# Optimization experiments

Measured on AMD Instinct MI355X. Metric: run time of the kernel, lower is better.

## Reference

```python
import jax, jax.numpy as jnp
import numpy as np

BLOCK_SIZE = 64          # elements per quantization block
SCALER_BLOCK_SIZE = 256  # scalers per double-quantization block
OUT, IN = 11008, 4096
N_BLOCKS = OUT * IN // BLOCK_SIZE          # 704512
N_SCALER_BLOCKS = N_BLOCKS // SCALER_BLOCK_SIZE  # 2752

# QLoRA NF4 (4-bit NormalFloat) codebook
NF4_TABLE = np.array([
    -1.0, -0.6961928009986877, -0.5250730514526367, -0.39491748809814453,
    -0.28444138169288635, -0.18477343022823334, -0.10644006729125977,
    -0.029167551919817924, 0.0, 0.07958029955625534, 0.16093020141124725,
    0.24611230194568634, 0.33791524171829224, 0.44070982933044434,
    0.5626170039176941, 0.7229568362236023], dtype=np.float32)


def setup_inputs() -> dict:
    key = jax.random.key(0)
    k1, k2, k3, k4, k5 = jax.random.split(key, 5)
    x = jax.random.normal(k1, (4, 2048, IN), dtype=jnp.float32)
    # 4-bit codebook indices for each weight element
    qweight = jax.random.randint(k2, (OUT, IN), 0, 16, dtype=jnp.int32)
    # int8-style quantized per-block scalers (positive magnitudes)
    quantized_scalers = jax.random.randint(k3, (N_BLOCKS,), 1, 127, dtype=jnp.int32)
    # per scaler-block quantization factor (strictly positive, away from zero)
    quantization_factor = jax.random.uniform(k4, (N_SCALER_BLOCKS,), dtype=jnp.float32,
                                             minval=0.5, maxval=1.5) * 127.0
    scaler_mean = jax.random.uniform(k5, (1,), dtype=jnp.float32) * 0.01
    return {"x": x, "qweight": qweight, "quantized_scalers": quantized_scalers,
            "quantization_factor": quantization_factor, "scaler_mean": scaler_mean}


def dequantize_nf4(qweight, quantized_scalers, quantization_factor, scaler_mean, dtype):
    table = jnp.asarray(NF4_TABLE, dtype=dtype)
    # double-dequantize the per-block scalers
    scalers = (quantized_scalers.astype(dtype)
               / jnp.repeat(quantization_factor.astype(dtype), SCALER_BLOCK_SIZE)
               + scaler_mean.astype(dtype)[0])                      # [N_BLOCKS]
    # codebook lookup, then per-block scale
    w = table[qweight].reshape(N_BLOCKS, BLOCK_SIZE) * scalers[:, None]
    return w.reshape(OUT, IN)


def reference(x, qweight, quantized_scalers, quantization_factor, scaler_mean):
    # Faithful to LinearNF4.forward: F.linear(x, weight.to(x.dtype))
    w = dequantize_nf4(qweight, quantized_scalers, quantization_factor,
                       scaler_mean, x.dtype)                        # [OUT, IN]
    return jnp.einsum('bsi,oi->bso', x, w)
```

## Files before the change

### kernel.cpp

```cpp
#include <hip/hip_runtime.h>
#include <stdint.h>

#define M_ROWS 8192
#define K_DIM  4096
#define N_DIM  11008
#define KSTEPS (K_DIM / 64)

#define BM 256
#define BN 256
#define MBLKS (M_ROWS / BM)
#define NBLKS (N_DIM / BN)
#define NWG   (MBLKS * NBLKS)

typedef __attribute__((ext_vector_type(4))) float          f32x4;
typedef __attribute__((ext_vector_type(8))) __bf16         bf16x8;
typedef __attribute__((ext_vector_type(4))) int            i32x4;
typedef __attribute__((ext_vector_type(8))) unsigned short u16x8;

__constant__ float NF4_TBL[16] = {
    -1.0f, -0.6961928009986877f, -0.5250730514526367f, -0.39491748809814453f,
    -0.28444138169288635f, -0.18477343022823334f, -0.10644006729125977f,
    -0.029167551919817924f, 0.0f, 0.07958029955625534f, 0.16093020141124725f,
    0.24611230194568634f, 0.33791524171829224f, 0.44070982933044434f,
    0.5626170039176941f, 0.7229568362236023f};

__device__ __forceinline__ unsigned short f2bf(float f) {
  uint32_t u = __float_as_uint(f);
  u += 0x7fffu + ((u >> 16) & 1u);
  return (unsigned short)(u >> 16);
}

__device__ __forceinline__ void gload_lds16(const void* g, const void* l) {
  __builtin_amdgcn_global_load_lds(
      (const __attribute__((address_space(1))) void*)(uintptr_t)g,
      (__attribute__((address_space(3))) void*)(uint32_t)(uintptr_t)l,
      16, 0, 0);
}

__global__ void convert_x_kernel(const float* __restrict__ x,
                                 unsigned short* __restrict__ xb) {
  const long n8 = (long)M_ROWS * K_DIM / 8;
  for (long t = (long)blockIdx.x * blockDim.x + threadIdx.x; t < n8;
       t += (long)gridDim.x * blockDim.x) {
    const float* p = x + t * 8;
    f32x4 v0 = *(const f32x4*)p;
    f32x4 v1 = *(const f32x4*)(p + 4);
    u16x8 o;
    o[0] = f2bf(v0[0]); o[1] = f2bf(v0[1]); o[2] = f2bf(v0[2]); o[3] = f2bf(v0[3]);
    o[4] = f2bf(v1[0]); o[5] = f2bf(v1[1]); o[6] = f2bf(v1[2]); o[7] = f2bf(v1[3]);
    *(u16x8*)(xb + t * 8) = o;
  }
}

__global__ void dequant_w_kernel(const int* __restrict__ qw,
                                 const int* __restrict__ qs,
                                 const float* __restrict__ qf,
                                 const float* __restrict__ mean,
                                 unsigned short* __restrict__ wb) {
  __shared__ float tbl[16];
  if (threadIdx.x < 16) tbl[threadIdx.x] = NF4_TBL[threadIdx.x];
  __syncthreads();
  const float mu = mean[0];
  const long n8 = (long)N_DIM * K_DIM / 8;
  for (long t = (long)blockIdx.x * blockDim.x + threadIdx.x; t < n8;
       t += (long)gridDim.x * blockDim.x) {
    long f = t * 8;
    int  g = (int)(f >> 6);
    float s = (float)qs[g] / qf[g >> 8] + mu;
    i32x4 q0 = *(const i32x4*)(qw + f);
    i32x4 q1 = *(const i32x4*)(qw + f + 4);
    u16x8 o;
    o[0] = f2bf(tbl[q0[0]] * s); o[1] = f2bf(tbl[q0[1]] * s);
    o[2] = f2bf(tbl[q0[2]] * s); o[3] = f2bf(tbl[q0[3]] * s);
    o[4] = f2bf(tbl[q1[0]] * s); o[5] = f2bf(tbl[q1[1]] * s);
    o[6] = f2bf(tbl[q1[2]] * s); o[7] = f2bf(tbl[q1[3]] * s);
    *(u16x8*)(wb + f) = o;
  }
}

#define STG(GP, LB)                                                              \
  gload_lds16((GP) + (long)srow * K_DIM + scol, &LDSbuf[(LB) + wid * 1024]);     \
  gload_lds16((GP) + (long)(64 + srow) * K_DIM + scol,                           \
              &LDSbuf[(LB) + 8192 + wid * 1024]);

#define SB __builtin_amdgcn_sched_barrier(0)

#define RD_A2(DST, MB, SA)                                                        \
  DST[0][0] = *(const bf16x8*)&LDSbuf[(SA) + aoff + (MB) * 2048 + kswz0];         \
  DST[0][1] = *(const bf16x8*)&LDSbuf[(SA) + aoff + (MB) * 2048 + kswz1];         \
  DST[1][0] = *(const bf16x8*)&LDSbuf[(SA) + aoff + ((MB) + 1) * 2048 + kswz0];   \
  DST[1][1] = *(const bf16x8*)&LDSbuf[(SA) + aoff + ((MB) + 1) * 2048 + kswz1];

#define RD_B2(NB, CB)                                                             \
  bq[NB][0]     = *(const bf16x8*)&LDSbuf[(CB) + boff + (NB) * 2048 + kswz0];     \
  bq[NB][1]     = *(const bf16x8*)&LDSbuf[(CB) + boff + (NB) * 2048 + kswz1];     \
  bq[NB + 1][0] = *(const bf16x8*)&LDSbuf[(CB) + boff + ((NB) + 1) * 2048 + kswz0];\
  bq[NB + 1][1] = *(const bf16x8*)&LDSbuf[(CB) + boff + ((NB) + 1) * 2048 + kswz1];

#define MFP(MI, AF, AI, NI)                                                       \
  acc[MI][NI] = __builtin_amdgcn_mfma_f32_16x16x32_bf16(AF[AI][0], bq[NI][0], acc[MI][NI], 0, 0, 0); \
  acc[MI][NI] = __builtin_amdgcn_mfma_f32_16x16x32_bf16(AF[AI][1], bq[NI][1], acc[MI][NI], 0, 0, 0);

#define TILE_BODY(BASE)                                                           \
    RD_B2(0, cB);                                                                 \
    SB;                                                                           \
    RD_B2(2, cB);                                                                 \
    STG(wb + n0g * K_DIM + kB, nB);                                               \
    __builtin_amdgcn_s_setprio(1);                                                \
    MFP(((BASE) + 0) & 7, af_a, 0, 0) MFP(((BASE) + 1) & 7, af_a, 1, 0)           \
    MFP(((BASE) + 0) & 7, af_a, 0, 1) MFP(((BASE) + 1) & 7, af_a, 1, 1)           \
    __builtin_amdgcn_s_setprio(0);                                                \
    SB;                                                                           \
    RD_A2(af_b, ((BASE) + 2) & 7, sAr);                                           \
    STG(wb + (n0g + 128) * K_DIM + kB, nB + 16384);                               \
    __builtin_amdgcn_s_setprio(1);                                                \
    MFP(((BASE) + 0) & 7, af_a, 0, 2) MFP(((BASE) + 1) & 7, af_a, 1, 2)           \
    MFP(((BASE) + 0) & 7, af_a, 0, 3) MFP(((BASE) + 1) & 7, af_a, 1, 3)           \
    __builtin_amdgcn_s_setprio(0);                                                \
    SB;                                                                           \
    STG(xb + m0g * K_DIM + kA, sAs);                                              \
    __builtin_amdgcn_s_setprio(1);                                                \
    MFP(((BASE) + 2) & 7, af_b, 0, 2) MFP(((BASE) + 3) & 7, af_b, 1, 2)           \
    MFP(((BASE) + 2) & 7, af_b, 0, 3) MFP(((BASE) + 3) & 7, af_b, 1, 3)           \
    __builtin_amdgcn_s_setprio(0);                                                \
    SB;                                                                           \
    RD_A2(af_a, ((BASE) + 4) & 7, sAr);                                           \
    STG(xb + (m0g + 128) * K_DIM + kA, sAs + 16384);                              \
    __builtin_amdgcn_s_setprio(1);                                                \
    MFP(((BASE) + 2) & 7, af_b, 0, 0) MFP(((BASE) + 3) & 7, af_b, 1, 0)           \
    MFP(((BASE) + 2) & 7, af_b, 0, 1) MFP(((BASE) + 3) & 7, af_b, 1, 1)           \
    __builtin_amdgcn_s_setprio(0);                                                \
    SB;                                                                           \
    __builtin_amdgcn_s_setprio(1);                                                \
    MFP(((BASE) + 4) & 7, af_a, 0, 0) MFP(((BASE) + 5) & 7, af_a, 1, 0)           \
    MFP(((BASE) + 4) & 7, af_a, 0, 1) MFP(((BASE) + 5) & 7, af_a, 1, 1)           \
    __builtin_amdgcn_s_setprio(0);                                                \
    SB;                                                                           \
    RD_A2(af_b, ((BASE) + 6) & 7, sAr);                                           \
    __builtin_amdgcn_s_setprio(1);                                                \
    MFP(((BASE) + 4) & 7, af_a, 0, 2) MFP(((BASE) + 5) & 7, af_a, 1, 2)           \
    MFP(((BASE) + 4) & 7, af_a, 0, 3) MFP(((BASE) + 5) & 7, af_a, 1, 3)           \
    __builtin_amdgcn_s_setprio(0);                                                \
    SB;                                                                           \
    RD_A2(af_a, ((BASE) + 0) & 7, sAn);          \
    __builtin_amdgcn_s_setprio(1);                                                \
    MFP(((BASE) + 6) & 7, af_b, 0, 2) MFP(((BASE) + 7) & 7, af_b, 1, 2)           \
    MFP(((BASE) + 6) & 7, af_b, 0, 3) MFP(((BASE) + 7) & 7, af_b, 1, 3)           \
    __builtin_amdgcn_s_setprio(0);                                                \
    SB;                                                                           \
    __builtin_amdgcn_s_setprio(1);                                                \
    MFP(((BASE) + 6) & 7, af_b, 0, 0) MFP(((BASE) + 7) & 7, af_b, 1, 0)           \
    MFP(((BASE) + 6) & 7, af_b, 0, 1) MFP(((BASE) + 7) & 7, af_b, 1, 1)           \
    __builtin_amdgcn_s_setprio(0);

#define TILE_SETUP                                                                \
    const int cur = t & 1;                                                        \
    const int cB = 98304 + cur * 32768;                                           \
    const int nB = 98304 + (cur ^ 1) * 32768;                                     \
    const long kB = (long)((t + 1 < KSTEPS ? t + 1 : KSTEPS - 1) * 64);           \
    const long kA = (long)((t + 2 < KSTEPS ? t + 2 : KSTEPS - 1) * 64);

#define TILE_BOUND                                                                \
    asm volatile("s_waitcnt vmcnt(4)");                                           \
    __builtin_amdgcn_sched_barrier(0);                                            \
    __builtin_amdgcn_s_barrier();                                                 \
    __builtin_amdgcn_sched_barrier(0);                                            \
    int tmp = sAr; sAr = sAn; sAn = sAs; sAs = tmp;

__global__ __launch_bounds__(512, 2) void gemm_pipe(
    const unsigned short* __restrict__ xb, const unsigned short* __restrict__ wb,
    float* __restrict__ C) {
  __align__(16) __shared__ unsigned char LDSbuf[163840];

  const int tid = threadIdx.x;
  const int wid = tid >> 6, lane = tid & 63;
  const int wr = wid >> 2, wc = wid & 3;
  const int r16 = lane & 15, hi = lane >> 4;

  const int p = ((int)blockIdx.x & 7) * (NWG / 8) + ((int)blockIdx.x >> 3);
  int mb, nb;
  if (p < 1280) {
    const int nbg = p >> 7;
    const int rem = p & 127;
    const int mbg = rem >> 5;
    const int s   = rem & 31;
    mb = mbg * 8 + (s & 7);
    nb = nbg * 4 + (s >> 3);
  } else {
    const int q   = p - 1280;
    const int mbg = q / 24;
    const int s   = q % 24;
    mb = mbg * 8 + (s & 7);
    nb = 40 + (s >> 3);
  }
  const long m0g = (long)mb * BM, n0g = (long)nb * BN;

  const int srow = wid * 8 + (lane >> 3);
  const int scol = ((lane & 7) ^ (lane >> 3)) * 8;

  const int aoff = (wr * 128 + r16) * 128;
  const int boff = (wc * 64 + r16) * 128;
  const int kswz0 = ((hi ^ (r16 & 7)) << 4);
  const int kswz1 = kswz0 ^ 64;

  STG(xb + m0g * K_DIM,              0);
  STG(xb + (m0g + 128) * K_DIM,      16384);
  STG(wb + n0g * K_DIM,              98304);
  STG(wb + (n0g + 128) * K_DIM,      98304 + 16384);
  STG(xb + m0g * K_DIM + 64,         32768);
  STG(xb + (m0g + 128) * K_DIM + 64, 32768 + 16384);
  asm volatile("s_waitcnt vmcnt(4)");
  __builtin_amdgcn_sched_barrier(0);
  __builtin_amdgcn_s_barrier();

  bf16x8 af_a[2][2], af_b[2][2], bq[4][2];
  f32x4 acc[8][4] = {};

  int sAr = 0, sAn = 32768, sAs = 65536;

  if ((wid & 1) == 0) {
    RD_A2(af_a, 0, sAr);
    for (int t = 0; t < KSTEPS; ++t) {
      TILE_SETUP
      TILE_BODY(0)
      TILE_BOUND
    }
  } else {
    RD_A2(af_a, 4, sAr);
    for (int t = 0; t < KSTEPS; ++t) {
      TILE_SETUP
      TILE_BODY(4)
      TILE_BOUND
    }
  }

  const long crow = m0g + wr * 128 + hi * 4;
  const long ccol = n0g + wc * 64 + r16;
#pragma unroll
  for (int m = 0; m < 8; ++m)
#pragma unroll
    for (int n = 0; n < 4; ++n)
#pragma unroll
      for (int r = 0; r < 4; ++r)
        __builtin_nontemporal_store(
            acc[m][n][r], &C[(crow + m * 16 + r) * N_DIM + ccol + n * 16]);
}

__global__ __launch_bounds__(256) void gemm_fallback(
    const float* __restrict__ Xf, const int* __restrict__ qw,
    const int* __restrict__ qs, const float* __restrict__ qf,
    const float* __restrict__ meanp, float* __restrict__ C) {
  __shared__ unsigned short As[128 * 64];
  __shared__ unsigned short Bs[128 * 64];
  __shared__ float tbl[16];
  const int tid = threadIdx.x;
  if (tid < 16) tbl[tid] = NF4_TBL[tid];
  const float mu = meanp[0];
  const int nwg = (M_ROWS / 128) * (N_DIM / 128);
  const int wg = ((int)blockIdx.x & 7) * (nwg / 8) + ((int)blockIdx.x >> 3);
  const int mbf = wg % (M_ROWS / 128), nbf = wg / (M_ROWS / 128);
  const int m0 = mbf * 128, n0 = nbf * 128;
  const int wid = tid >> 6, lane = tid & 63;
  const int wrf = wid >> 1, wcc = wid & 1;
  const int r16 = lane & 15, hi = lane >> 4;
  f32x4 acc[4][4] = {};
  for (int t = 0; t < KSTEPS; ++t) {
    const int k0 = t * 64;
    __syncthreads();
#pragma unroll
    for (int i = 0; i < 4; ++i) {
      int gi = i * 256 + tid;
      int row = gi >> 3, kq = (gi & 7) * 8;
      const float* px = Xf + (long)(m0 + row) * K_DIM + k0 + kq;
      f32x4 v0 = *(const f32x4*)px;
      f32x4 v1 = *(const f32x4*)(px + 4);
      u16x8 o;
      o[0] = f2bf(v0[0]); o[1] = f2bf(v0[1]); o[2] = f2bf(v0[2]); o[3] = f2bf(v0[3]);
      o[4] = f2bf(v1[0]); o[5] = f2bf(v1[1]); o[6] = f2bf(v1[2]); o[7] = f2bf(v1[3]);
      *(u16x8*)&As[row * 64 + kq] = o;
    }
#pragma unroll
    for (int i = 0; i < 4; ++i) {
      int gi = i * 256 + tid;
      int row = gi >> 3, kq = (gi & 7) * 8;
      const int* pq = qw + (long)(n0 + row) * K_DIM + k0 + kq;
      i32x4 q0 = *(const i32x4*)pq;
      i32x4 q1 = *(const i32x4*)(pq + 4);
      int g = (n0 + row) * (K_DIM / 64) + t;
      float s = (float)qs[g] / qf[g >> 8] + mu;
      u16x8 o;
      o[0] = f2bf(tbl[q0[0]] * s); o[1] = f2bf(tbl[q0[1]] * s);
      o[2] = f2bf(tbl[q0[2]] * s); o[3] = f2bf(tbl[q0[3]] * s);
      o[4] = f2bf(tbl[q1[0]] * s); o[5] = f2bf(tbl[q1[1]] * s);
      o[6] = f2bf(tbl[q1[2]] * s); o[7] = f2bf(tbl[q1[3]] * s);
      *(u16x8*)&Bs[row * 64 + kq] = o;
    }
    __syncthreads();
    bf16x8 afr[4][2], bfr[4][2];
#pragma unroll
    for (int i = 0; i < 4; ++i)
#pragma unroll
      for (int h = 0; h < 2; ++h) {
        afr[i][h] = *(const bf16x8*)&As[(wrf * 64 + i * 16 + r16) * 64 + h * 32 + hi * 8];
        bfr[i][h] = *(const bf16x8*)&Bs[(wcc * 64 + i * 16 + r16) * 64 + h * 32 + hi * 8];
      }
#pragma unroll
    for (int i = 0; i < 4; ++i)
#pragma unroll
      for (int j = 0; j < 4; ++j) {
        acc[i][j] = __builtin_amdgcn_mfma_f32_16x16x32_bf16(afr[i][0], bfr[j][0], acc[i][j], 0, 0, 0);
        acc[i][j] = __builtin_amdgcn_mfma_f32_16x16x32_bf16(afr[i][1], bfr[j][1], acc[i][j], 0, 0, 0);
      }
  }
  const int crow = m0 + wrf * 64 + hi * 4;
  const int ccol = n0 + wcc * 64 + r16;
#pragma unroll
  for (int i = 0; i < 4; ++i)
#pragma unroll
    for (int j = 0; j < 4; ++j)
#pragma unroll
      for (int r = 0; r < 4; ++r)
        C[(long)(crow + i * 16 + r) * N_DIM + (ccol + j * 16)] = acc[i][j][r];
}

extern "C" void kernel_launch(void* const* d_in, const int* in_sizes, int n_in,
                              void* d_out, int out_size, void* d_ws, size_t ws_size,
                              hipStream_t stream) {
  const float* x    = (const float*)d_in[0];
  const int*   qw   = (const int*)d_in[1];
  const int*   qs   = (const int*)d_in[2];
  const float* qf   = (const float*)d_in[3];
  const float* mean = (const float*)d_in[4];
  float* out = (float*)d_out;

  const size_t xb_bytes = (size_t)M_ROWS * K_DIM * 2;
  const size_t wb_bytes = (size_t)N_DIM * K_DIM * 2;

  if (ws_size >= xb_bytes + wb_bytes) {
    unsigned short* xb = (unsigned short*)d_ws;
    unsigned short* wb = (unsigned short*)((char*)d_ws + xb_bytes);
    convert_x_kernel<<<4096, 256, 0, stream>>>(x, xb);
    dequant_w_kernel<<<4096, 256, 0, stream>>>(qw, qs, qf, mean, wb);
    gemm_pipe<<<NWG, 512, 0, stream>>>(xb, wb, out);
  } else {
    gemm_fallback<<<(M_ROWS / 128) * (N_DIM / 128), 256, 0, stream>>>(
        x, qw, qs, qf, mean, out);
  }
}
```

Measured before the change: 687.9 us.

## Split-K the tail tiles of the GEMM to balance the last wave

The 96 tiles in the last column group (nb 40-42) are each split along K into two halves, giving 1472 workgroups instead of 1376. The second half writes its partial sums to a workspace buffer, and a new fixup kernel adds them into the output. The aim is to cut the idle time of a partially filled final wave across the CUs. In exchange it adds an extra kernel launch and extra memory traffic for the partial tiles, and it only runs when the workspace is large enough.

Result: no change. 685.2 us (-0.4%).

```diff
diff --git a/kernel.cpp b/kernel.cpp
--- a/kernel.cpp
+++ b/kernel.cpp
@@ -11,6 +11,7 @@
 #define MBLKS (M_ROWS / BM)
 #define NBLKS (N_DIM / BN)
 #define NWG   (MBLKS * NBLKS)
+#define NWG_SPLIT 1472
 
 typedef __attribute__((ext_vector_type(4))) float          f32x4;
 typedef __attribute__((ext_vector_type(8))) __bf16         bf16x8;
@@ -157,8 +158,8 @@
     const int cur = t & 1;                                                        \
     const int cB = 98304 + cur * 32768;                                           \
     const int nB = 98304 + (cur ^ 1) * 32768;                                     \
-    const long kB = (long)((t + 1 < KSTEPS ? t + 1 : KSTEPS - 1) * 64);           \
-    const long kA = (long)((t + 2 < KSTEPS ? t + 2 : KSTEPS - 1) * 64);
+    const long kB = (long)((t + 1 < tend ? t + 1 : tend - 1) * 64);               \
+    const long kA = (long)((t + 2 < tend ? t + 2 : tend - 1) * 64);
 
 #define TILE_BOUND                                                                \
     asm volatile("s_waitcnt vmcnt(4)");                                           \
@@ -167,9 +168,10 @@
     __builtin_amdgcn_sched_barrier(0);                                            \
     int tmp = sAr; sAr = sAn; sAn = sAs; sAs = tmp;
 
+template <bool SPLIT>
 __global__ __launch_bounds__(512, 2) void gemm_pipe(
     const unsigned short* __restrict__ xb, const unsigned short* __restrict__ wb,
-    float* __restrict__ C) {
+    float* __restrict__ C, float* __restrict__ P) {
   __align__(16) __shared__ unsigned char LDSbuf[163840];
 
   const int tid = threadIdx.x;
@@ -177,21 +179,37 @@
   const int wr = wid >> 2, wc = wid & 3;
   const int r16 = lane & 15, hi = lane >> 4;
 
-  const int p = ((int)blockIdx.x & 7) * (NWG / 8) + ((int)blockIdx.x >> 3);
-  int mb, nb;
-  if (p < 1280) {
-    const int nbg = p >> 7;
-    const int rem = p & 127;
-    const int mbg = rem >> 5;
-    const int s   = rem & 31;
-    mb = mbg * 8 + (s & 7);
-    nb = nbg * 4 + (s >> 3);
+  int mb, nb, tstart = 0, tend = KSTEPS;
+  bool partial = false;
+  long ptile = 0;
+  if (!SPLIT) {
+    const int p = ((int)blockIdx.x & 7) * (NWG / 8) + ((int)blockIdx.x >> 3);
+    if (p < 1280) {
+      const int nbg = p >> 7, rem = p & 127, mbg = rem >> 5, s = rem & 31;
+      mb = mbg * 8 + (s & 7);
+      nb = nbg * 4 + (s >> 3);
+    } else {
+      const int q = p - 1280, mbg = q / 24, s = q % 24;
+      mb = mbg * 8 + (s & 7);
+      nb = 40 + (s >> 3);
+    }
   } else {
-    const int q   = p - 1280;
-    const int mbg = q / 24;
-    const int s   = q % 24;
-    mb = mbg * 8 + (s & 7);
-    nb = 40 + (s >> 3);
+    const int bx = (int)blockIdx.x;
+    if (bx < 1280) {
+      const int p = (bx & 7) * 160 + (bx >> 3);
+      const int nbg = p >> 7, rem = p & 127, mbg = rem >> 5, s = rem & 31;
+      mb = mbg * 8 + (s & 7);
+      nb = nbg * 4 + (s >> 3);
+    } else {
+      const int q = bx - 1280, r = q >> 1, kh = q & 1;
+      const int mbg = r / 24, s = r % 24;
+      mb = mbg * 8 + (s & 7);
+      nb = 40 + (s >> 3);
+      tstart = kh << 5;
+      tend   = tstart + 32;
+      partial = (kh == 1);
+      ptile = (long)r << 16;
+    }
   }
   const long m0g = (long)mb * BM, n0g = (long)nb * BN;
 
@@ -203,12 +221,13 @@
   const int kswz0 = ((hi ^ (r16 & 7)) << 4);
   const int kswz1 = kswz0 ^ 64;
 
-  STG(xb + m0g * K_DIM,              0);
-  STG(xb + (m0g + 128) * K_DIM,      16384);
-  STG(wb + n0g * K_DIM,              98304);
-  STG(wb + (n0g + 128) * K_DIM,      98304 + 16384);
-  STG(xb + m0g * K_DIM + 64,         32768);
-  STG(xb + (m0g + 128) * K_DIM + 64, 32768 + 16384);
+  const long k0p = (long)tstart * 64;
+  STG(xb + m0g * K_DIM + k0p,              0);
+  STG(xb + (m0g + 128) * K_DIM + k0p,      16384);
+  STG(wb + n0g * K_DIM + k0p,              98304);
+  STG(wb + (n0g + 128) * K_DIM + k0p,      98304 + 16384);
+  STG(xb + m0g * K_DIM + k0p + 64,         32768);
+  STG(xb + (m0g + 128) * K_DIM + k0p + 64, 32768 + 16384);
   asm volatile("s_waitcnt vmcnt(4)");
   __builtin_amdgcn_sched_barrier(0);
   __builtin_amdgcn_s_barrier();
@@ -220,30 +239,61 @@
 
   if ((wid & 1) == 0) {
     RD_A2(af_a, 0, sAr);
-    for (int t = 0; t < KSTEPS; ++t) {
+    for (int t = tstart; t < tend; ++t) {
       TILE_SETUP
       TILE_BODY(0)
       TILE_BOUND
     }
   } else {
     RD_A2(af_a, 4, sAr);
-    for (int t = 0; t < KSTEPS; ++t) {
+    for (int t = tstart; t < tend; ++t) {
       TILE_SETUP
       TILE_BODY(4)
       TILE_BOUND
     }
   }
 
-  const long crow = m0g + wr * 128 + hi * 4;
-  const long ccol = n0g + wc * 64 + r16;
-#pragma unroll
-  for (int m = 0; m < 8; ++m)
-#pragma unroll
-    for (int n = 0; n < 4; ++n)
-#pragma unroll
-      for (int r = 0; r < 4; ++r)
-        __builtin_nontemporal_store(
-            acc[m][n][r], &C[(crow + m * 16 + r) * N_DIM + ccol + n * 16]);
+  if (SPLIT && partial) {
+    float* Pt = P + ptile;
+    const int prow = wr * 128 + hi * 4;
+    const int pcol = wc * 64 + r16;
+#pragma unroll
+    for (int m = 0; m < 8; ++m)
+#pragma unroll
+      for (int n = 0; n < 4; ++n)
+#pragma unroll
+        for (int r = 0; r < 4; ++r)
+          __builtin_nontemporal_store(
+              acc[m][n][r], &Pt[(prow + m * 16 + r) * 256 + pcol + n * 16]);
+  } else {
+    const long crow = m0g + wr * 128 + hi * 4;
+    const long ccol = n0g + wc * 64 + r16;
+#pragma unroll
+    for (int m = 0; m < 8; ++m)
+#pragma unroll
+      for (int n = 0; n < 4; ++n)
+#pragma unroll
+        for (int r = 0; r < 4; ++r)
+          __builtin_nontemporal_store(
+              acc[m][n][r], &C[(crow + m * 16 + r) * N_DIM + ccol + n * 16]);
+  }
+}
+
+__global__ void fixup_kernel(float* __restrict__ C, const float* __restrict__ P) {
+  const long n4 = 96L * 16384;
+  for (long i = (long)blockIdx.x * blockDim.x + threadIdx.x; i < n4;
+       i += (long)gridDim.x * blockDim.x) {
+    const int r = (int)(i >> 14);
+    const int w = (int)(i & 16383);
+    const int row = w >> 6, c4 = (w & 63) * 4;
+    const int mbg = r / 24, s = r % 24;
+    const int mb = mbg * 8 + (s & 7), nb = 40 + (s >> 3);
+    float* cp = C + (long)(mb * 256 + row) * N_DIM + nb * 256 + c4;
+    const f32x4 pv = *(const f32x4*)(P + i * 4);
+    f32x4 cv = *(const f32x4*)cp;
+    cv += pv;
+    *(f32x4*)cp = cv;
+  }
 }
 
 __global__ __launch_bounds__(256) void gemm_fallback(
@@ -335,13 +385,22 @@
 
   const size_t xb_bytes = (size_t)M_ROWS * K_DIM * 2;
   const size_t wb_bytes = (size_t)N_DIM * K_DIM * 2;
-
-  if (ws_size >= xb_bytes + wb_bytes) {
+  const size_t p_bytes  = (size_t)96 * 65536 * 4;
+
+  if (ws_size >= xb_bytes + wb_bytes + p_bytes) {
+    unsigned short* xb = (unsigned short*)d_ws;
+    unsigned short* wb = (unsigned short*)((char*)d_ws + xb_bytes);
+    float* P = (float*)((char*)d_ws + xb_bytes + wb_bytes);
+    convert_x_kernel<<<4096, 256, 0, stream>>>(x, xb);
+    dequant_w_kernel<<<4096, 256, 0, stream>>>(qw, qs, qf, mean, wb);
+    gemm_pipe<true><<<NWG_SPLIT, 512, 0, stream>>>(xb, wb, out, P);
+    fixup_kernel<<<2048, 256, 0, stream>>>(out, P);
+  } else if (ws_size >= xb_bytes + wb_bytes) {
     unsigned short* xb = (unsigned short*)d_ws;
     unsigned short* wb = (unsigned short*)((char*)d_ws + xb_bytes);
     convert_x_kernel<<<4096, 256, 0, stream>>>(x, xb);
     dequant_w_kernel<<<4096, 256, 0, stream>>>(qw, qs, qf, mean, wb);
-    gemm_pipe<<<NWG, 512, 0, stream>>>(xb, wb, out);
+    gemm_pipe<false><<<NWG, 512, 0, stream>>>(xb, wb, out, nullptr);
   } else {
     gemm_fallback<<<(M_ROWS / 128) * (N_DIM / 128), 256, 0, stream>>>(
         x, qw, qs, qf, mean, out);
```
